# Kernel tuning notes

Measured on AMD Instinct MI355X. Metric: run time of the kernel, lower is better.

The kernel has to match this reference:

```python
import jax, jax.numpy as jnp
import numpy as np
from jax import lax

V, D, H, C = 32000, 300, 300, 3
B, T = 128, 512


def setup_inputs() -> dict:
    key = jax.random.key(0)
    ks = jax.random.split(key, 8)
    sentence_ids = jax.random.randint(ks[0], (B, T), 0, V, dtype=jnp.int32)
    lengths = jnp.maximum(jax.random.randint(ks[1], (B,), 0, T, dtype=jnp.int32), 1)
    labels = jax.random.randint(ks[2], (B,), 0, C, dtype=jnp.int32)
    embedding = jax.random.normal(ks[3], (V, D), jnp.float32) * 0.1
    W_lstm = jax.random.normal(ks[4], (D + H, 4 * H), jnp.float32) * 0.05
    b_lstm = jnp.zeros((4 * H,), jnp.float32)
    W_dense = jax.random.normal(ks[5], (H, C), jnp.float32) * 0.05
    b_dense = jnp.zeros((C,), jnp.float32)
    return {"sentence_ids": sentence_ids, "lengths": lengths, "labels": labels,
            "embedding": embedding, "W_lstm": W_lstm, "b_lstm": b_lstm,
            "W_dense": W_dense, "b_dense": b_dense}


def reference(sentence_ids, lengths, labels, embedding, W_lstm, b_lstm, W_dense, b_dense):
    # Embedding lookup: [B, T, D]
    x = embedding[sentence_ids]
    b, t, d = x.shape
    h_units = W_dense.shape[0]
    FORGET_BIAS = 1.0  # TF BasicLSTMCell default

    xs = jnp.swapaxes(x, 0, 1)                                   # [T, B, D]
    step_mask = (jnp.arange(t)[:, None] < lengths[None, :])      # [T, B]

    def step(carry, inp):
        h, c = carry
        xt, m = inp                                              # [B,D], [B]
        z = jnp.concatenate([xt, h], axis=-1) @ W_lstm + b_lstm  # [B, 4H]
        i, j, f, o = jnp.split(z, 4, axis=-1)
        new_c = c * jax.nn.sigmoid(f + FORGET_BIAS) + jax.nn.sigmoid(i) * jnp.tanh(j)
        new_h = jnp.tanh(new_c) * jax.nn.sigmoid(o)
        mm = m[:, None]
        # dynamic_rnn: freeze state past each sequence's length
        h = jnp.where(mm, new_h, h)
        c = jnp.where(mm, new_c, c)
        return (h, c), None

    h0 = jnp.zeros((b, h_units), x.dtype)
    c0 = jnp.zeros((b, h_units), x.dtype)
    (h_final, _), _ = lax.scan(step, (h0, c0), (xs, step_mask))

    logits = h_final @ W_dense + b_dense                          # [B, C]
    logp = jax.nn.log_softmax(logits, axis=-1)
    nll = -jnp.take_along_axis(logp, labels[:, None].astype(jnp.int32), axis=1)[:, 0]
    loss = jnp.mean(nll)
    return loss, logits
```

## Files before the change

### kernel.cpp

```cpp
#include <hip/hip_runtime.h>
#include <hip/hip_bf16.h>
#include <math.h>

#define VV   32000
#define DD   300
#define HU   300
#define NC   3
#define BB   128
#define TT   512
#define N4H  1200
#define CHUNK 64
#define NCHUNK (TT / CHUNK)

#define GC   15
#define GR   16
#define RPW  8
#define UPW  20
#define KSW  96
#define HLB_STRIDE 312
#define HLB_SIZE   (16 * HLB_STRIDE + 32)

static constexpr size_t ZX_F    = (size_t)BB * CHUNK * N4H;
static constexpr size_t EX_W    = (size_t)2 * GR * RPW * HU;
static constexpr size_t CST_F   = (size_t)BB * HU;
static constexpr size_t HFIN_F  = (size_t)BB * HU;
static constexpr size_t EMB16_W = (size_t)VV * 320;
static constexpr size_t WT_W    = (size_t)N4H * 320;

typedef __attribute__((ext_vector_type(8))) short bf16x8;
typedef __attribute__((ext_vector_type(8))) _Float16 f16x8;
typedef __attribute__((ext_vector_type(4))) float f32x4;
typedef unsigned long long ull;

__device__ __forceinline__ short f2bf(float f) {
    unsigned u = __float_as_uint(f);
    u += 0x7fff + ((u >> 16) & 1);
    return (short)(u >> 16);
}
__device__ __forceinline__ short f2h(float f) {
    _Float16 h = (_Float16)f;
    return *(short*)&h;
}
__device__ __forceinline__ float h2f(short s) {
    _Float16 h = *(_Float16*)&s;
    return (float)h;
}
__device__ __forceinline__ float sigm(float x) { return 1.f / (1.f + __expf(-x)); }
__device__ __forceinline__ float tanh_(float x) { return 1.f - 2.f / (__expf(2.f * x) + 1.f); }

__global__ void init_kernel(ull* __restrict__ ex, float* __restrict__ cst,
                            float* __restrict__ out) {
    size_t i = (size_t)blockIdx.x * 256 + threadIdx.x;
    if (i < EX_W) ex[i] = 0ull;
    if (i < CST_F) cst[i] = 0.f;
    if (i == 0) out[0] = 0.f;
}

__global__ void prep_kernel(const float* __restrict__ emb,
                            const float* __restrict__ Wl,
                            short* __restrict__ emb16, short* __restrict__ wt) {
    const int NE = VV * 40;
    const int NW = N4H * 40;
    for (int j = blockIdx.x * 256 + threadIdx.x; j < NE + NW;
         j += gridDim.x * 256) {
        if (j < NE) {
            int v = j / 40, kb = (j % 40) * 8;
            bf16x8 o;
            if (kb + 8 <= DD) {
                const float* s = emb + (size_t)v * DD + kb;
                float4 a = *(const float4*)s, b = *(const float4*)(s + 4);
                o[0] = f2bf(a.x); o[1] = f2bf(a.y); o[2] = f2bf(a.z); o[3] = f2bf(a.w);
                o[4] = f2bf(b.x); o[5] = f2bf(b.y); o[6] = f2bf(b.z); o[7] = f2bf(b.w);
            } else {
                #pragma unroll
                for (int e = 0; e < 8; ++e) {
                    int k = kb + e;
                    o[e] = (k < DD) ? f2bf(emb[(size_t)v * DD + k]) : (short)0;
                }
            }
            *(bf16x8*)&emb16[(size_t)v * 320 + kb] = o;
        } else {
            int jj = j - NE;
            int col = jj / 40, kb = (jj % 40) * 8;
            bf16x8 o;
            #pragma unroll
            for (int e = 0; e < 8; ++e) {
                int k = kb + e;
                o[e] = (k < DD) ? f2bf(Wl[(size_t)k * N4H + col]) : (short)0;
            }
            *(bf16x8*)&wt[(size_t)col * 320 + kb] = o;
        }
    }
}

__global__ __launch_bounds__(256) void zx_gemm(
    const short* __restrict__ emb16, const int* __restrict__ ids,
    const short* __restrict__ wt, const float* __restrict__ bl,
    float* __restrict__ zx, int t0)
{
    __shared__ short A_l[256 * 40];

    const int tid = threadIdx.x;
    const int m0  = blockIdx.x * 256;
    const int n0  = blockIdx.y * 80;
    const int wv  = tid >> 6, ln = tid & 63;

    int myid;
    {
        int m = m0 + tid;
        int b = m >> 6, tc = m & (CHUNK - 1);
        myid = ids[b * TT + t0 + tc];
    }
    const short* arow = emb16 + (size_t)myid * 320;

    f32x4 acc[4][5];
    for (int i = 0; i < 4; ++i)
        for (int j = 0; j < 5; ++j)
            acc[i][j] = (f32x4){0.f, 0.f, 0.f, 0.f};

    for (int k0 = 0; k0 < 320; k0 += 32) {
        __syncthreads();
        {
            #pragma unroll
            for (int q = 0; q < 4; ++q)
                *(bf16x8*)&A_l[tid * 40 + q * 8] =
                    *(const bf16x8*)(arow + k0 + q * 8);
        }
        __syncthreads();
        const int koff = (ln >> 4) * 8;
        bf16x8 afr[4], bfr[5];
        #pragma unroll
        for (int mt = 0; mt < 4; ++mt) {
            int row = wv * 64 + mt * 16 + (ln & 15);
            afr[mt] = *(const bf16x8*)&A_l[row * 40 + koff];
        }
        #pragma unroll
        for (int nt = 0; nt < 5; ++nt) {
            int col = n0 + nt * 16 + (ln & 15);
            bfr[nt] = *(const bf16x8*)&wt[(size_t)col * 320 + k0 + koff];
        }
        #pragma unroll
        for (int mt = 0; mt < 4; ++mt)
            #pragma unroll
            for (int nt = 0; nt < 5; ++nt)
                acc[mt][nt] = __builtin_amdgcn_mfma_f32_16x16x32_bf16(
                    afr[mt], bfr[nt], acc[mt][nt], 0, 0, 0);
    }
    #pragma unroll
    for (int mt = 0; mt < 4; ++mt) {
        #pragma unroll
        for (int nt = 0; nt < 5; ++nt) {
            #pragma unroll
            for (int rg = 0; rg < 4; ++rg) {
                int row = m0 + wv * 64 + mt * 16 + (ln >> 4) * 4 + rg;
                int col = n0 + nt * 16 + (ln & 15);
                zx[(size_t)row * N4H + col] = acc[mt][nt][rg] + bl[col];
            }
        }
    }
}

__global__ __launch_bounds__(256, 1) void lstm_rec(
    const float* __restrict__ zx, const float* __restrict__ Wl,
    const int* __restrict__ lens, ull* __restrict__ ex,
    float* __restrict__ cst, float* __restrict__ hfin, int t0)
{
    const int tid = threadIdx.x;
    const int wv  = tid >> 6, ln = tid & 63;
    const int rg  = blockIdx.x % GR;
    const int cgi = blockIdx.x / GR;
    const int r0  = rg * RPW;
    const int u0  = cgi * UPW;
    const int m   = ln & 15;
    const int quad = ln >> 4;

    const int pstart_tbl[4] = {0, 4, 9, 14};
    const int np_tbl[4]     = {5, 6, 6, 1};
    const int pstart = pstart_tbl[wv];
    const int np     = np_tbl[wv];

    __shared__ short h_hi[HLB_SIZE];
    __shared__ short h_lo[HLB_SIZE];
    __shared__ float zp[2][4][RPW][84];
    __shared__ short w_l[4 * 15 * 64 * 8];

    #pragma unroll
    for (int s = 0; s < 3; ++s) {
        #pragma unroll
        for (int nt = 0; nt < 5; ++nt) {
            int c    = nt * 16 + m;
            int gate = c / 20;
            int wcol = 300 * gate + u0 + (c % 20);
            f16x8 b;
            #pragma unroll
            for (int j = 0; j < 8; ++j) {
                int k = KSW * wv + 32 * s + quad * 8 + j;
                float v = (k < HU) ? Wl[(size_t)(DD + k) * N4H + wcol] : 0.f;
                b[j] = (_Float16)v;
            }
            *(f16x8*)&w_l[(((wv * 15) + (s * 5 + nt)) * 64 + ln) * 8] = b;
        }
    }
    const int nks = (wv == 3) ? 1 : 3;

    for (int i = tid; i < HLB_SIZE; i += 256) { h_hi[i] = 0; h_lo[i] = 0; }

    const int g_u = tid % UPW, g_r = tid / UPW;
    const bool gl = (tid < RPW * UPW);
    float c_reg = 0.f, ho_reg = 0.f;
    int mylen = 0;
    if (gl) {
        c_reg = cst[(size_t)(r0 + g_r) * HU + u0 + g_u];
        mylen = lens[r0 + g_r];
        if (t0 > 0) {
            ull v = __hip_atomic_load(
                ex + (((size_t)(t0 & 1) * GR + rg) * RPW + g_r) * HU + u0 + g_u,
                __ATOMIC_RELAXED, __HIP_MEMORY_SCOPE_AGENT);
            unsigned d = (unsigned)v;
            ho_reg = h2f((short)(d & 0xFFFFu)) + h2f((short)(d >> 16));
        }
    }
    __syncthreads();

    for (int tc = 0; tc < CHUNK; ++tc) {
        const int t = t0 + tc;
        const int par = t & 1;

        float z_pre[4];
        if (gl) {
            const float* zrow = zx + ((size_t)(r0 + g_r) * CHUNK + tc) * N4H;
            #pragma unroll
            for (int gg = 0; gg < 4; ++gg)
                z_pre[gg] = zrow[300 * gg + u0 + g_u];
        }

        if (t > 0) {
            const ull* exb = ex + ((size_t)par * GR + rg) * (RPW * HU);

            if (ln < np) {
                const ull* sp = exb + (pstart + ln) * UPW;
                while ((int)(__hip_atomic_load(sp, __ATOMIC_RELAXED,
                             __HIP_MEMORY_SCOPE_AGENT) >> 32) < t)
                    __builtin_amdgcn_s_sleep(1);
            }

            if (wv < 3) {
                unsigned pend = 0xFFFu;
                do {
                    ull v[12];
                    #pragma unroll
                    for (int k = 0; k < 12; ++k)
                        if ((pend >> k) & 1) {
                            int i = ln + (k << 6);
                            int r = i / 96, u = KSW * wv + (i % 96);
                            v[k] = __hip_atomic_load(exb + r * HU + u,
                                                     __ATOMIC_RELAXED,
                                                     __HIP_MEMORY_SCOPE_AGENT);
                        }
                    unsigned got = 0;
                    #pragma unroll
                    for (int k = 0; k < 12; ++k) {
                        if (((pend >> k) & 1) && (int)(v[k] >> 32) >= t) {
                            int i = ln + (k << 6);
                            int r = i / 96, u = KSW * wv + (i % 96);
                            int idx = r * HLB_STRIDE + u;
                            unsigned d = (unsigned)v[k];
                            h_hi[idx] = (short)(d & 0xFFFFu);
                            h_lo[idx] = (short)(d >> 16);
                            got |= 1u << k;
                        }
                    }
                    pend &= ~got;
                    if (pend) __builtin_amdgcn_s_sleep(1);
                } while (pend);
            } else {
                unsigned pend = (ln < 32) ? 0x3u : 0x1u;
                do {
                    ull v[2];
                    #pragma unroll
                    for (int k = 0; k < 2; ++k)
                        if ((pend >> k) & 1) {
                            int i = ln + (k << 6);
                            int r = i / 12, u = 288 + (i % 12);
                            v[k] = __hip_atomic_load(exb + r * HU + u,
                                                     __ATOMIC_RELAXED,
                                                     __HIP_MEMORY_SCOPE_AGENT);
                        }
                    unsigned got = 0;
                    #pragma unroll
                    for (int k = 0; k < 2; ++k) {
                        if (((pend >> k) & 1) && (int)(v[k] >> 32) >= t) {
                            int i = ln + (k << 6);
                            int r = i / 12, u = 288 + (i % 12);
                            int idx = r * HLB_STRIDE + u;
                            unsigned d = (unsigned)v[k];
                            h_hi[idx] = (short)(d & 0xFFFFu);
                            h_lo[idx] = (short)(d >> 16);
                            got |= 1u << k;
                        }
                    }
                    pend &= ~got;
                    if (pend) __builtin_amdgcn_s_sleep(1);
                } while (pend);
            }
        }

        f32x4 acc[5];
        #pragma unroll
        for (int nt = 0; nt < 5; ++nt) acc[nt] = (f32x4){0.f, 0.f, 0.f, 0.f};
        for (int s = 0; s < nks; ++s) {
            const int aoff = m * HLB_STRIDE + KSW * wv + 32 * s + quad * 8;
            f16x8 ah = *(const f16x8*)&h_hi[aoff];
            f16x8 al = *(const f16x8*)&h_lo[aoff];
            f16x8 bfr[5];
            #pragma unroll
            for (int nt = 0; nt < 5; ++nt)
                bfr[nt] = *(const f16x8*)&w_l[(((wv * 15) + (s * 5 + nt)) * 64 + ln) * 8];
            #pragma unroll
            for (int nt = 0; nt < 5; ++nt)
                acc[nt] = __builtin_amdgcn_mfma_f32_16x16x32_f16(
                    ah, bfr[nt], acc[nt], 0, 0, 0);
            #pragma unroll
            for (int nt = 0; nt < 5; ++nt)
                acc[nt] = __builtin_amdgcn_mfma_f32_16x16x32_f16(
                    al, bfr[nt], acc[nt], 0, 0, 0);
        }
        if (ln < 32) {
            #pragma unroll
            for (int nt = 0; nt < 5; ++nt)
                #pragma unroll
                for (int r4 = 0; r4 < 4; ++r4)
                    zp[par][wv][quad * 4 + r4][nt * 16 + m] = acc[nt][r4];
        }
        __syncthreads();

        if (gl) {
            const int b = r0 + g_r;
            float z4[4];
            #pragma unroll
            for (int gg = 0; gg < 4; ++gg) {
                int cidx = gg * UPW + g_u;
                z4[gg] = z_pre[gg] + zp[par][0][g_r][cidx] + zp[par][1][g_r][cidx]
                                   + zp[par][2][g_r][cidx] + zp[par][3][g_r][cidx];
            }
            float ig = sigm(z4[0]);
            float jg = tanh_(z4[1]);
            float fg = sigm(z4[2] + 1.0f);
            float og = sigm(z4[3]);
            float c_new = c_reg * fg + ig * jg;
            float h_new = tanh_(c_new) * og;
            bool upd = (t < mylen);
            ho_reg = upd ? h_new : ho_reg;
            c_reg  = upd ? c_new : c_reg;
            short hhi = f2h(ho_reg);
            short hlo = f2h(ho_reg - h2f(hhi));
            ull pk = ((ull)(unsigned)(t + 1) << 32)
                   | ((ull)(unsigned short)hlo << 16) | (ull)(unsigned short)hhi;
            __hip_atomic_store(
                ex + (((size_t)((t + 1) & 1) * GR + rg) * RPW + g_r) * HU + u0 + g_u,
                pk, __ATOMIC_RELAXED, __HIP_MEMORY_SCOPE_AGENT);
            if (tc == CHUNK - 1) hfin[(size_t)b * HU + u0 + g_u] = ho_reg;
        }
    }
    if (gl) cst[(size_t)(r0 + g_r) * HU + u0 + g_u] = c_reg;
}

__global__ __launch_bounds__(64) void cls_kernel(
    const float* __restrict__ hfin, const float* __restrict__ Wd,
    const float* __restrict__ bd, const int* __restrict__ labels,
    float* __restrict__ out)
{
    const int b = blockIdx.x;
    const int ln = threadIdx.x;
    const float* h = hfin + (size_t)b * HU;
    float p0 = 0.f, p1 = 0.f, p2 = 0.f;
    for (int k = ln; k < HU; k += 64) {
        float hv = h[k];
        p0 += hv * Wd[k * 3 + 0];
        p1 += hv * Wd[k * 3 + 1];
        p2 += hv * Wd[k * 3 + 2];
    }
    #pragma unroll
    for (int off = 32; off > 0; off >>= 1) {
        p0 += __shfl_down(p0, off);
        p1 += __shfl_down(p1, off);
        p2 += __shfl_down(p2, off);
    }
    if (ln == 0) {
        float l0 = p0 + bd[0], l1 = p1 + bd[1], l2 = p2 + bd[2];
        float m = fmaxf(l0, fmaxf(l1, l2));
        float lse = m + logf(__expf(l0 - m) + __expf(l1 - m) + __expf(l2 - m));
        int lab = labels[b];
        float sel = (lab == 0) ? l0 : ((lab == 1) ? l1 : l2);
        float nll = lse - sel;
        out[1 + b * 3 + 0] = l0;
        out[1 + b * 3 + 1] = l1;
        out[1 + b * 3 + 2] = l2;
        atomicAdd(out, nll * (1.0f / BB));
    }
}

extern "C" void kernel_launch(void* const* d_in, const int* in_sizes, int n_in,
                              void* d_out, int out_size, void* d_ws, size_t ws_size,
                              hipStream_t stream) {
    const int*   ids  = (const int*)d_in[0];
    const int*   lens = (const int*)d_in[1];
    const int*   labs = (const int*)d_in[2];
    const float* emb  = (const float*)d_in[3];
    const float* Wl   = (const float*)d_in[4];
    const float* bl   = (const float*)d_in[5];
    const float* Wd   = (const float*)d_in[6];
    const float* bd   = (const float*)d_in[7];
    float* out = (float*)d_out;

    float* zx    = (float*)d_ws;
    ull*   ex    = (ull*)(zx + ZX_F);
    float* cst   = (float*)(ex + EX_W);
    float* hfin  = cst + CST_F;
    short* emb16 = (short*)(hfin + HFIN_F);
    short* wt    = emb16 + EMB16_W;

    {
        int n = (int)((EX_W + 255) / 256);
        init_kernel<<<n, 256, 0, stream>>>(ex, cst, out);
    }
    prep_kernel<<<2048, 256, 0, stream>>>(emb, Wl, emb16, wt);

    for (int c = 0; c < NCHUNK; ++c) {
        int t0 = c * CHUNK;
        zx_gemm<<<dim3(32, 15), 256, 0, stream>>>(emb16, ids, wt, bl, zx, t0);
        lstm_rec<<<GR * GC, 256, 0, stream>>>(zx, Wl, lens, ex, cst, hfin, t0);
    }
    cls_kernel<<<BB, 64, 0, stream>>>(hfin, Wd, bd, labs, out);
}
```

Baseline: 2.226 ms.

## Compute full-sequence input projections in one GEMM when workspace allows

When the workspace is large enough to hold the input projection for all 512 timesteps, the code runs one zx_gemm over the whole sequence and one persistent lstm_rec launch covering every step. This replaces eight alternating GEMM/recurrence launch pairs, removing launch gaps and the recurrence drain and refill at each chunk boundary. The cost is a much larger zx buffer (about 315 MB) that is written once and streamed back, and the path silently falls back to chunking if the workspace is too small.

```diff
diff --git a/kernel.cpp b/kernel.cpp
--- a/kernel.cpp
+++ b/kernel.cpp
@@ -20,7 +20,8 @@
 #define HLB_STRIDE 312
 #define HLB_SIZE   (16 * HLB_STRIDE + 32)
 
-static constexpr size_t ZX_F    = (size_t)BB * CHUNK * N4H;
+static constexpr size_t ZX_CHUNK_F = (size_t)BB * CHUNK * N4H;
+static constexpr size_t ZX_FULL_F  = (size_t)BB * TT * N4H;
 static constexpr size_t EX_W    = (size_t)2 * GR * RPW * HU;
 static constexpr size_t CST_F   = (size_t)BB * HU;
 static constexpr size_t HFIN_F  = (size_t)BB * HU;
@@ -96,7 +97,7 @@
 __global__ __launch_bounds__(256) void zx_gemm(
     const short* __restrict__ emb16, const int* __restrict__ ids,
     const short* __restrict__ wt, const float* __restrict__ bl,
-    float* __restrict__ zx, int t0)
+    float* __restrict__ zx, int t0, int sdbits)
 {
     __shared__ short A_l[256 * 40];
 
@@ -108,7 +109,7 @@
     int myid;
     {
         int m = m0 + tid;
-        int b = m >> 6, tc = m & (CHUNK - 1);
+        int b = m >> sdbits, tc = m & ((1 << sdbits) - 1);
         myid = ids[b * TT + t0 + tc];
     }
     const short* arow = emb16 + (size_t)myid * 320;
@@ -163,7 +164,8 @@
 __global__ __launch_bounds__(256, 1) void lstm_rec(
     const float* __restrict__ zx, const float* __restrict__ Wl,
     const int* __restrict__ lens, ull* __restrict__ ex,
-    float* __restrict__ cst, float* __restrict__ hfin, int t0)
+    float* __restrict__ cst, float* __restrict__ hfin,
+    int t0, int nsteps, int sdbits)
 {
     const int tid = threadIdx.x;
     const int wv  = tid >> 6, ln = tid & 63;
@@ -222,13 +224,14 @@
     }
     __syncthreads();
 
-    for (int tc = 0; tc < CHUNK; ++tc) {
+    for (int tc = 0; tc < nsteps; ++tc) {
         const int t = t0 + tc;
         const int par = t & 1;
 
         float z_pre[4];
         if (gl) {
-            const float* zrow = zx + ((size_t)(r0 + g_r) * CHUNK + tc) * N4H;
+            const float* zrow = zx
+                + (((size_t)(r0 + g_r) << sdbits) + tc) * N4H;
             #pragma unroll
             for (int gg = 0; gg < 4; ++gg)
                 z_pre[gg] = zrow[300 * gg + u0 + g_u];
@@ -359,7 +362,7 @@
             __hip_atomic_store(
                 ex + (((size_t)((t + 1) & 1) * GR + rg) * RPW + g_r) * HU + u0 + g_u,
                 pk, __ATOMIC_RELAXED, __HIP_MEMORY_SCOPE_AGENT);
-            if (tc == CHUNK - 1) hfin[(size_t)b * HU + u0 + g_u] = ho_reg;
+            if (tc == nsteps - 1) hfin[(size_t)b * HU + u0 + g_u] = ho_reg;
         }
     }
     if (gl) cst[(size_t)(r0 + g_r) * HU + u0 + g_u] = c_reg;
@@ -413,8 +416,13 @@
     const float* bd   = (const float*)d_in[7];
     float* out = (float*)d_out;
 
+    const size_t tail_f = (size_t)(EX_W * 2) + CST_F + HFIN_F
+                        + (EMB16_W + WT_W + 1) / 2;
+    const bool full = ws_size >= (ZX_FULL_F + tail_f + 1024) * sizeof(float);
+    const size_t zxf = full ? ZX_FULL_F : ZX_CHUNK_F;
+
     float* zx    = (float*)d_ws;
-    ull*   ex    = (ull*)(zx + ZX_F);
+    ull*   ex    = (ull*)(zx + zxf);
     float* cst   = (float*)(ex + EX_W);
     float* hfin  = cst + CST_F;
     short* emb16 = (short*)(hfin + HFIN_F);
@@ -426,10 +434,19 @@
     }
     prep_kernel<<<2048, 256, 0, stream>>>(emb, Wl, emb16, wt);
 
-    for (int c = 0; c < NCHUNK; ++c) {
-        int t0 = c * CHUNK;
-        zx_gemm<<<dim3(32, 15), 256, 0, stream>>>(emb16, ids, wt, bl, zx, t0);
-        lstm_rec<<<GR * GC, 256, 0, stream>>>(zx, Wl, lens, ex, cst, hfin, t0);
+    if (full) {
+        zx_gemm<<<dim3((BB * TT) / 256, 15), 256, 0, stream>>>(
+            emb16, ids, wt, bl, zx, 0, 9);
+        lstm_rec<<<GR * GC, 256, 0, stream>>>(zx, Wl, lens, ex, cst, hfin,
+                                              0, TT, 9);
+    } else {
+        for (int c = 0; c < NCHUNK; ++c) {
+            int t0 = c * CHUNK;
+            zx_gemm<<<dim3((BB * CHUNK) / 256, 15), 256, 0, stream>>>(
+                emb16, ids, wt, bl, zx, t0, 6);
+            lstm_rec<<<GR * GC, 256, 0, stream>>>(zx, Wl, lens, ex, cst, hfin,
+                                                  t0, CHUNK, 6);
+        }
     }
     cls_kernel<<<BB, 64, 0, stream>>>(hfin, Wd, bd, labs, out);
 }
```

New measurement: 2.211 ms. Within noise of the previous version (-0.7%).

## Fuse input projection into recurrent kernel with prefetched embedding rows

Applied to the files above, without the earlier changes.

Removes the separate chunked zx GEMM and instead computes each step's x@W_x contribution inside the persistent LSTM kernel, using bf16 MFMAs on embedding rows staged into double-buffered shared memory and loaded one step ahead. The per-step gate preactivation no longer reads a large fp32 zx buffer from global memory, and the eight kernel launches per pair collapse into one launch covering all 512 steps. The trade-off is extra MFMA work and gather latency on the serial critical path of every step, plus more shared memory and registers for the resident input weights.

```diff
diff --git a/kernel.cpp b/kernel.cpp
--- a/kernel.cpp
+++ b/kernel.cpp
@@ -9,8 +9,6 @@
 #define BB   128
 #define TT   512
 #define N4H  1200
-#define CHUNK 64
-#define NCHUNK (TT / CHUNK)
 
 #define GC   15
 #define GR   16
@@ -19,8 +17,8 @@
 #define KSW  96
 #define HLB_STRIDE 312
 #define HLB_SIZE   (16 * HLB_STRIDE + 32)
-
-static constexpr size_t ZX_F    = (size_t)BB * CHUNK * N4H;
+#define XST  328
+
 static constexpr size_t EX_W    = (size_t)2 * GR * RPW * HU;
 static constexpr size_t CST_F   = (size_t)BB * HU;
 static constexpr size_t HFIN_F  = (size_t)BB * HU;
@@ -93,77 +91,12 @@
     }
 }
 
-__global__ __launch_bounds__(256) void zx_gemm(
-    const short* __restrict__ emb16, const int* __restrict__ ids,
-    const short* __restrict__ wt, const float* __restrict__ bl,
-    float* __restrict__ zx, int t0)
-{
-    __shared__ short A_l[256 * 40];
-
-    const int tid = threadIdx.x;
-    const int m0  = blockIdx.x * 256;
-    const int n0  = blockIdx.y * 80;
-    const int wv  = tid >> 6, ln = tid & 63;
-
-    int myid;
-    {
-        int m = m0 + tid;
-        int b = m >> 6, tc = m & (CHUNK - 1);
-        myid = ids[b * TT + t0 + tc];
-    }
-    const short* arow = emb16 + (size_t)myid * 320;
-
-    f32x4 acc[4][5];
-    for (int i = 0; i < 4; ++i)
-        for (int j = 0; j < 5; ++j)
-            acc[i][j] = (f32x4){0.f, 0.f, 0.f, 0.f};
-
-    for (int k0 = 0; k0 < 320; k0 += 32) {
-        __syncthreads();
-        {
-            #pragma unroll
-            for (int q = 0; q < 4; ++q)
-                *(bf16x8*)&A_l[tid * 40 + q * 8] =
-                    *(const bf16x8*)(arow + k0 + q * 8);
-        }
-        __syncthreads();
-        const int koff = (ln >> 4) * 8;
-        bf16x8 afr[4], bfr[5];
-        #pragma unroll
-        for (int mt = 0; mt < 4; ++mt) {
-            int row = wv * 64 + mt * 16 + (ln & 15);
-            afr[mt] = *(const bf16x8*)&A_l[row * 40 + koff];
-        }
-        #pragma unroll
-        for (int nt = 0; nt < 5; ++nt) {
-            int col = n0 + nt * 16 + (ln & 15);
-            bfr[nt] = *(const bf16x8*)&wt[(size_t)col * 320 + k0 + koff];
-        }
-        #pragma unroll
-        for (int mt = 0; mt < 4; ++mt)
-            #pragma unroll
-            for (int nt = 0; nt < 5; ++nt)
-                acc[mt][nt] = __builtin_amdgcn_mfma_f32_16x16x32_bf16(
-                    afr[mt], bfr[nt], acc[mt][nt], 0, 0, 0);
-    }
-    #pragma unroll
-    for (int mt = 0; mt < 4; ++mt) {
-        #pragma unroll
-        for (int nt = 0; nt < 5; ++nt) {
-            #pragma unroll
-            for (int rg = 0; rg < 4; ++rg) {
-                int row = m0 + wv * 64 + mt * 16 + (ln >> 4) * 4 + rg;
-                int col = n0 + nt * 16 + (ln & 15);
-                zx[(size_t)row * N4H + col] = acc[mt][nt][rg] + bl[col];
-            }
-        }
-    }
-}
-
 __global__ __launch_bounds__(256, 1) void lstm_rec(
-    const float* __restrict__ zx, const float* __restrict__ Wl,
-    const int* __restrict__ lens, ull* __restrict__ ex,
-    float* __restrict__ cst, float* __restrict__ hfin, int t0)
+    const short* __restrict__ emb16, const short* __restrict__ wt,
+    const int* __restrict__ ids, const float* __restrict__ bl,
+    const float* __restrict__ Wl, const int* __restrict__ lens,
+    ull* __restrict__ ex, float* __restrict__ cst, float* __restrict__ hfin,
+    int t0, int nsteps)
 {
     const int tid = threadIdx.x;
     const int wv  = tid >> 6, ln = tid & 63;
@@ -181,8 +114,11 @@
 
     __shared__ short h_hi[HLB_SIZE];
     __shared__ short h_lo[HLB_SIZE];
+    __shared__ short x_l[2][16 * XST];
     __shared__ float zp[2][4][RPW][84];
     __shared__ short w_l[4 * 15 * 64 * 8];
+
+    const int nks = (wv == 3) ? 1 : 3;
 
     #pragma unroll
     for (int s = 0; s < 3; ++s) {
@@ -201,17 +137,32 @@
             *(f16x8*)&w_l[(((wv * 15) + (s * 5 + nt)) * 64 + ln) * 8] = b;
         }
     }
-    const int nks = (wv == 3) ? 1 : 3;
+
+    bf16x8 bxr[15];
+    for (int s = 0; s < nks; ++s) {
+        #pragma unroll
+        for (int nt = 0; nt < 5; ++nt) {
+            int c    = nt * 16 + m;
+            int gate = c / 20;
+            int wcol = 300 * gate + u0 + (c % 20);
+            bxr[s * 5 + nt] = *(const bf16x8*)
+                &wt[(size_t)wcol * 320 + KSW * wv + 32 * s + quad * 8];
+        }
+    }
 
     for (int i = tid; i < HLB_SIZE; i += 256) { h_hi[i] = 0; h_lo[i] = 0; }
+    for (int i = tid; i < 2 * 16 * XST; i += 256) ((short*)x_l)[i] = 0;
 
     const int g_u = tid % UPW, g_r = tid / UPW;
     const bool gl = (tid < RPW * UPW);
-    float c_reg = 0.f, ho_reg = 0.f;
+    float c_reg = 0.f, ho_reg = 0.f, bl_c[4];
     int mylen = 0;
     if (gl) {
         c_reg = cst[(size_t)(r0 + g_r) * HU + u0 + g_u];
         mylen = lens[r0 + g_r];
+        #pragma unroll
+        for (int gg = 0; gg < 4; ++gg)
+            bl_c[gg] = bl[gg * HU + u0 + g_u];
         if (t0 > 0) {
             ull v = __hip_atomic_load(
                 ex + (((size_t)(t0 & 1) * GR + rg) * RPW + g_r) * HU + u0 + g_u,
@@ -220,18 +171,36 @@
             ho_reg = h2f((short)(d & 0xFFFFu)) + h2f((short)(d >> 16));
         }
     }
+
+    const int xr0 = tid / 40,        xq0 = tid - xr0 * 40;
+    const int xr1 = (tid + 256) / 40, xq1 = (tid + 256) - xr1 * 40;
+    const size_t ido0 = (size_t)(r0 + xr0) * TT;
+    const size_t ido1 = (size_t)(r0 + xr1) * TT;
+    const int xd0 = xr0 * XST + xq0 * 8;
+    const int xd1 = xr1 * XST + xq1 * 8;
+
     __syncthreads();
 
-    for (int tc = 0; tc < CHUNK; ++tc) {
+    {
+        bf16x8 v0 = *(const bf16x8*)(emb16 + (size_t)ids[ido0 + t0] * 320 + xq0 * 8);
+        *(bf16x8*)&x_l[t0 & 1][xd0] = v0;
+        if (tid < 64) {
+            bf16x8 v1 = *(const bf16x8*)(emb16 + (size_t)ids[ido1 + t0] * 320 + xq1 * 8);
+            *(bf16x8*)&x_l[t0 & 1][xd1] = v1;
+        }
+    }
+    __syncthreads();
+
+    for (int tc = 0; tc < nsteps; ++tc) {
         const int t = t0 + tc;
         const int par = t & 1;
 
-        float z_pre[4];
-        if (gl) {
-            const float* zrow = zx + ((size_t)(r0 + g_r) * CHUNK + tc) * N4H;
-            #pragma unroll
-            for (int gg = 0; gg < 4; ++gg)
-                z_pre[gg] = zrow[300 * gg + u0 + g_u];
+        bf16x8 xg0, xg1;
+        const bool stg = (tc + 1 < nsteps);
+        if (stg) {
+            xg0 = *(const bf16x8*)(emb16 + (size_t)ids[ido0 + t + 1] * 320 + xq0 * 8);
+            if (tid < 64)
+                xg1 = *(const bf16x8*)(emb16 + (size_t)ids[ido1 + t + 1] * 320 + xq1 * 8);
         }
 
         if (t > 0) {
@@ -309,9 +278,10 @@
         #pragma unroll
         for (int nt = 0; nt < 5; ++nt) acc[nt] = (f32x4){0.f, 0.f, 0.f, 0.f};
         for (int s = 0; s < nks; ++s) {
-            const int aoff = m * HLB_STRIDE + KSW * wv + 32 * s + quad * 8;
-            f16x8 ah = *(const f16x8*)&h_hi[aoff];
-            f16x8 al = *(const f16x8*)&h_lo[aoff];
+            const int ko = KSW * wv + 32 * s + quad * 8;
+            f16x8  ah = *(const f16x8*)&h_hi[m * HLB_STRIDE + ko];
+            f16x8  al = *(const f16x8*)&h_lo[m * HLB_STRIDE + ko];
+            bf16x8 ax = *(const bf16x8*)&x_l[par][m * XST + ko];
             f16x8 bfr[5];
             #pragma unroll
             for (int nt = 0; nt < 5; ++nt)
@@ -324,6 +294,10 @@
             for (int nt = 0; nt < 5; ++nt)
                 acc[nt] = __builtin_amdgcn_mfma_f32_16x16x32_f16(
                     al, bfr[nt], acc[nt], 0, 0, 0);
+            #pragma unroll
+            for (int nt = 0; nt < 5; ++nt)
+                acc[nt] = __builtin_amdgcn_mfma_f32_16x16x32_bf16(
+                    ax, bxr[s * 5 + nt], acc[nt], 0, 0, 0);
         }
         if (ln < 32) {
             #pragma unroll
@@ -332,6 +306,11 @@
                 for (int r4 = 0; r4 < 4; ++r4)
                     zp[par][wv][quad * 4 + r4][nt * 16 + m] = acc[nt][r4];
         }
+
+        if (stg) {
+            *(bf16x8*)&x_l[(t + 1) & 1][xd0] = xg0;
+            if (tid < 64) *(bf16x8*)&x_l[(t + 1) & 1][xd1] = xg1;
+        }
         __syncthreads();
 
         if (gl) {
@@ -340,8 +319,8 @@
             #pragma unroll
             for (int gg = 0; gg < 4; ++gg) {
                 int cidx = gg * UPW + g_u;
-                z4[gg] = z_pre[gg] + zp[par][0][g_r][cidx] + zp[par][1][g_r][cidx]
-                                   + zp[par][2][g_r][cidx] + zp[par][3][g_r][cidx];
+                z4[gg] = bl_c[gg] + zp[par][0][g_r][cidx] + zp[par][1][g_r][cidx]
+                                  + zp[par][2][g_r][cidx] + zp[par][3][g_r][cidx];
             }
             float ig = sigm(z4[0]);
             float jg = tanh_(z4[1]);
@@ -359,7 +338,7 @@
             __hip_atomic_store(
                 ex + (((size_t)((t + 1) & 1) * GR + rg) * RPW + g_r) * HU + u0 + g_u,
                 pk, __ATOMIC_RELAXED, __HIP_MEMORY_SCOPE_AGENT);
-            if (tc == CHUNK - 1) hfin[(size_t)b * HU + u0 + g_u] = ho_reg;
+            if (tc == nsteps - 1) hfin[(size_t)b * HU + u0 + g_u] = ho_reg;
         }
     }
     if (gl) cst[(size_t)(r0 + g_r) * HU + u0 + g_u] = c_reg;
@@ -413,8 +392,7 @@
     const float* bd   = (const float*)d_in[7];
     float* out = (float*)d_out;
 
-    float* zx    = (float*)d_ws;
-    ull*   ex    = (ull*)(zx + ZX_F);
+    ull*   ex    = (ull*)d_ws;
     float* cst   = (float*)(ex + EX_W);
     float* hfin  = cst + CST_F;
     short* emb16 = (short*)(hfin + HFIN_F);
@@ -426,10 +404,8 @@
     }
     prep_kernel<<<2048, 256, 0, stream>>>(emb, Wl, emb16, wt);
 
-    for (int c = 0; c < NCHUNK; ++c) {
-        int t0 = c * CHUNK;
-        zx_gemm<<<dim3(32, 15), 256, 0, stream>>>(emb16, ids, wt, bl, zx, t0);
-        lstm_rec<<<GR * GC, 256, 0, stream>>>(zx, Wl, lens, ex, cst, hfin, t0);
-    }
+    lstm_rec<<<GR * GC, 256, 0, stream>>>(emb16, wt, ids, bl, Wl, lens,
+                                          ex, cst, hfin, 0, TT);
+
     cls_kernel<<<BB, 64, 0, stream>>>(hfin, Wd, bd, labs, out);
 }
```

New measurement: 2.451 ms. 1.1x slower.
